# Optimization experiments

Measured on AMD Instinct MI355X. Metric: run time of the kernel, lower is better.

## Reference

```python
import jax, jax.numpy as jnp
import numpy as np

N_NODES = 50000
N_EDGES = 800000
IN_C = 128
OUT_C = 128


def setup_inputs() -> dict:
    key = jax.random.key(0)
    k1, k2, k3 = jax.random.split(key, 3)
    x = jax.random.normal(k1, (N_NODES, IN_C), dtype=jnp.float32)
    edge_index = jax.random.randint(k2, (2, N_EDGES), 0, N_NODES, dtype=jnp.int64)
    weight = jax.random.normal(k3, (IN_C, OUT_C), dtype=jnp.float32) * 0.01
    bias = jnp.zeros((OUT_C,), dtype=jnp.float32)
    return {"x": x, "edge_index": edge_index, "weight": weight, "bias": bias}


def reference(x, edge_index, weight, bias):
    num_nodes = x.shape[0]
    # add self-loops
    loop = jnp.arange(num_nodes, dtype=edge_index.dtype)
    src = jnp.concatenate([edge_index[0], loop])  # [E + N]
    dst = jnp.concatenate([edge_index[1], loop])  # [E + N]
    # in-degree (incl. self-loops) via scatter-add
    deg = jax.ops.segment_sum(jnp.ones_like(dst, dtype=x.dtype), dst,
                              num_segments=num_nodes)
    # deg >= 1 due to self-loops, but guard inf like the original
    deg_inv_sqrt = jnp.where(deg > 0, jax.lax.rsqrt(deg), 0.0)
    norm = deg_inv_sqrt[src] * deg_inv_sqrt[dst]  # [E + N]
    x_transformed = x @ weight  # [N, out_c]
    messages = x_transformed[src] * norm[:, None]  # [E + N, out_c]
    out = jax.ops.segment_sum(messages, dst, num_segments=num_nodes)
    return out + bias
```

## Files before the change

### kernel.cpp

```cpp
#include <hip/hip_runtime.h>

#define C 128
#define CHUNK 3200
#define SLOT 64
#define K4CAP 5120

typedef short bf16x8 __attribute__((ext_vector_type(8)));
typedef float f32x4 __attribute__((ext_vector_type(4)));

__device__ inline unsigned short f2bf(float f) {
    unsigned u = __float_as_uint(f);
    u += 0x7fffu + ((u >> 16) & 1u);
    return (unsigned short)(u >> 16);
}

__device__ inline unsigned pk2bf(float lo, float hi) {
    return (unsigned)f2bf(lo) | ((unsigned)f2bf(hi) << 16);
}

__global__ __launch_bounds__(256) void kA(
        const int* __restrict__ ei, int e,
        int* __restrict__ cnt, unsigned* __restrict__ staging,
        int nblocks, int nbuck,
        const float* __restrict__ W, unsigned short* __restrict__ Wt) {
    int b = blockIdx.x;
    int t = threadIdx.x;
    if (b >= nblocks) {
        int i = (b - nblocks) * 256 + t;
        int nn = i >> 7, k = i & 127;
        Wt[nn * 128 + k] = f2bf(W[k * 128 + nn]);
        return;
    }
    __shared__ int sdst[CHUNK];
    __shared__ int ssrc[CHUNK];
    __shared__ int h[256];
    __shared__ int c[256];
    h[t] = 0;
    __syncthreads();
    int base = b * CHUNK;
    int lim = min(CHUNK, e - base);
    for (int i = t; i < lim; i += 256) {
        int s = ei[base + i];
        int d = ei[e + base + i];
        ssrc[i] = s;
        sdst[i] = d;
        atomicAdd(&h[d >> 8], 1);
    }
    __syncthreads();
    if (t < nbuck) {
        cnt[t * nblocks + b] = h[t];
        c[t] = (t * nblocks + b) * SLOT;
    }
    __syncthreads();
    for (int i = t; i < lim; i += 256) {
        int s = ssrc[i];
        int d = sdst[i];
        int g = d >> 8;
        int pos = atomicAdd(&c[g], 1);
        if (pos < (g * nblocks + b + 1) * SLOT)
            staging[pos] = (unsigned)s | ((unsigned)(d & 255) << 16);
    }
}

__global__ __launch_bounds__(256) void kB(
        const unsigned* __restrict__ staging, const int* __restrict__ cnt,
        int nblocks, int nbuck,
        int2* __restrict__ row_se, float* __restrict__ dis,
        unsigned short* __restrict__ srcs,
        const float* __restrict__ x, const unsigned short* __restrict__ Wt,
        unsigned short* __restrict__ xts, int n) {
    __shared__ unsigned rec[K4CAP];
    __shared__ int sc[256];
    __shared__ int cu[256];
    int b = blockIdx.x, t = threadIdx.x;
    if (b < nbuck) {
        int g = b;
        int segc = (t < nblocks) ? cnt[g * nblocks + t] : 0;
        sc[t] = segc;
        __syncthreads();
        for (int off = 1; off < 256; off <<= 1) {
            int u = (t >= off) ? sc[t - off] : 0;
            __syncthreads();
            sc[t] += u;
            __syncthreads();
        }
        int segbase = sc[t] - segc;
        int total = min(sc[255], K4CAP);
        const unsigned* segp = staging + ((size_t)g * nblocks + t) * SLOT;
        for (int k = 0; k < segc; ++k)
            if (segbase + k < K4CAP) rec[segbase + k] = segp[k];
        __syncthreads();
        sc[t] = 0;
        __syncthreads();
        for (int li = t; li < total; li += 256)
            atomicAdd(&sc[rec[li] >> 16], 1);
        __syncthreads();
        int v = sc[t];
        __syncthreads();
        for (int off = 1; off < 256; off <<= 1) {
            int u = (t >= off) ? sc[t - off] : 0;
            __syncthreads();
            sc[t] += u;
            __syncthreads();
        }
        int excl = sc[t] - v;
        int idx = g * 256 + t;
        int s0 = g * K4CAP;
        if (idx < n) {
            row_se[idx] = make_int2(s0 + excl, s0 + excl + v);
            dis[idx] = rsqrtf((float)(v + 1));
        }
        cu[t] = s0 + excl;
        __syncthreads();
        for (int li = t; li < total; li += 256) {
            unsigned r = rec[li];
            int pos = atomicAdd(&cu[r >> 16], 1);
            srcs[pos] = (unsigned short)(r & 0xffffu);
        }
    } else {
        const int gb = b - nbuck;
        const int lane = t & 63;
        const int wave = t >> 6;
        const int m = lane & 15;
        const int q = lane >> 4;
        const int r0 = gb * 64 + wave * 16;
        const int row = r0 + m;
        const int rowc = (row < n) ? row : (n - 1);

        f32x4 acc[8];
#pragma unroll
        for (int nt = 0; nt < 8; ++nt) acc[nt] = (f32x4){0.f, 0.f, 0.f, 0.f};

#pragma unroll
        for (int kb = 0; kb < 4; ++kb) {
            const int k0 = kb * 32 + q * 8;
            const float4* xp = (const float4*)(x + (size_t)rowc * 128 + k0);
            float4 xa = xp[0];
            float4 xb = xp[1];
            union { unsigned u[4]; bf16x8 v; } af;
            af.u[0] = pk2bf(xa.x, xa.y);
            af.u[1] = pk2bf(xa.z, xa.w);
            af.u[2] = pk2bf(xb.x, xb.y);
            af.u[3] = pk2bf(xb.z, xb.w);
#pragma unroll
            for (int nt = 0; nt < 8; ++nt) {
                bf16x8 bf = *(const bf16x8*)(Wt + (size_t)(nt * 16 + m) * 128 + k0);
                acc[nt] = __builtin_amdgcn_mfma_f32_16x16x32_bf16(af.v, bf, acc[nt], 0, 0, 0);
            }
        }

#pragma unroll
        for (int nt = 0; nt < 8; ++nt) {
            int col = nt * 16 + m;
#pragma unroll
            for (int r = 0; r < 4; ++r) {
                int gr = r0 + q * 4 + r;
                if (gr < n)
                    xts[(size_t)gr * 128 + col] = f2bf(acc[nt][r]);
            }
        }
    }
}

__device__ inline void fma8(float* a, uint4 w, float d) {
    a[0] += __uint_as_float(w.x << 16) * d;
    a[1] += __uint_as_float(w.x & 0xffff0000u) * d;
    a[2] += __uint_as_float(w.y << 16) * d;
    a[3] += __uint_as_float(w.y & 0xffff0000u) * d;
    a[4] += __uint_as_float(w.z << 16) * d;
    a[5] += __uint_as_float(w.z & 0xffff0000u) * d;
    a[6] += __uint_as_float(w.w << 16) * d;
    a[7] += __uint_as_float(w.w & 0xffff0000u) * d;
}

__global__ void gather4(const int2* __restrict__ row_se,
                        const unsigned short* __restrict__ srcs,
                        const unsigned short* __restrict__ xts,
                        const float* __restrict__ dis,
                        const float* __restrict__ bias, float* __restrict__ out, int n) {
    int node = blockIdx.x * 4 + (threadIdx.x >> 6);
    if (node >= n) return;
    int lane = threadIdx.x & 63;
    int e = lane >> 4, q = lane & 15;
    const uint4* x4 = (const uint4*)xts;
    int2 se = row_se[node];
    int end = se.y;
    float dself = dis[node];
    float a0[8] = {0, 0, 0, 0, 0, 0, 0, 0};
    float a1[8] = {0, 0, 0, 0, 0, 0, 0, 0};
    if (e == 0) fma8(a0, x4[node * 16 + q], dself);
    int j = se.x + e;
    for (; j + 4 < end; j += 8) {
        int s0 = srcs[j], s1 = srcs[j + 4];
        float d0 = dis[s0], d1 = dis[s1];
        uint4 m0 = x4[s0 * 16 + q];
        uint4 m1 = x4[s1 * 16 + q];
        fma8(a0, m0, d0);
        fma8(a1, m1, d1);
    }
    if (j < end) {
        int s = srcs[j];
        fma8(a0, x4[s * 16 + q], dis[s]);
    }
#pragma unroll
    for (int i = 0; i < 8; ++i) a0[i] += a1[i];
#pragma unroll
    for (int i = 0; i < 8; ++i) {
        a0[i] += __shfl_xor(a0[i], 16, 64);
        a0[i] += __shfl_xor(a0[i], 32, 64);
    }
    if (e == 0) {
        const float4 b = ((const float4*)bias)[q * 2];
        float4 o;
        o.x = a0[0] * dself + b.x;
        o.y = a0[1] * dself + b.y;
        o.z = a0[2] * dself + b.z;
        o.w = a0[3] * dself + b.w;
        ((float4*)(out + (size_t)node * 128))[q * 2] = o;
    } else if (e == 1) {
        const float4 b = ((const float4*)bias)[q * 2 + 1];
        float4 o;
        o.x = a0[4] * dself + b.x;
        o.y = a0[5] * dself + b.y;
        o.z = a0[6] * dself + b.z;
        o.w = a0[7] * dself + b.w;
        ((float4*)(out + (size_t)node * 128))[q * 2 + 1] = o;
    }
}

extern "C" void kernel_launch(void* const* d_in, const int* in_sizes, int n_in,
                              void* d_out, int out_size, void* d_ws, size_t ws_size,
                              hipStream_t stream) {
    const float* x    = (const float*)d_in[0];
    const int*   ei   = (const int*)d_in[1];
    const float* W    = (const float*)d_in[2];
    const float* bias = (const float*)d_in[3];
    float* out = (float*)d_out;

    const int n = in_sizes[0] / C;
    const int e = in_sizes[1] / 2;
    const int nblocks = (e + CHUNK - 1) / CHUNK;
    const int nbuck = (n + 255) >> 8;
    const int G = (n + 63) / 64;

    char* p = (char*)d_ws;
    auto alloc = [&](size_t bytes) {
        char* r = p;
        p += (bytes + 15) & ~(size_t)15;
        return (void*)r;
    };
    int*      cnt     = (int*)alloc((size_t)nbuck * nblocks * 4);
    unsigned* staging = (unsigned*)alloc((size_t)nbuck * nblocks * SLOT * 4);
    int2*     row_se  = (int2*)alloc((size_t)n * 8);
    float*    dis     = (float*)alloc(n * 4);
    unsigned short* srcs = (unsigned short*)alloc((size_t)nbuck * K4CAP * 2);
    unsigned short* xts  = (unsigned short*)alloc((size_t)n * C * 2);
    unsigned short* Wt   = (unsigned short*)alloc(128 * 128 * 2);

    kA<<<nblocks + 64, 256, 0, stream>>>(ei, e, cnt, staging, nblocks, nbuck,
                                         W, Wt);
    kB<<<nbuck + G, 256, 0, stream>>>(staging, cnt, nblocks, nbuck, row_se,
                                      dis, srcs, x, Wt, xts, n);
    gather4<<<(n + 3) / 4, 256, 0, stream>>>(row_se, srcs, xts, dis, bias, out, n);
}
```

Before: 150.3 us.

## Move GEMM into first kernel with LDS-staged swizzled weights, split bucket finalize

The x@W GEMM blocks now run in the first launch alongside edge bucketing. Each GEMM block converts W to bf16 itself into a swizzled shared-memory tile, so the separate Wt global buffer and its dependency are gone. Bucket finalization becomes its own small kernel that reads staging with vectorized uint4 loads and clamps counts to SLOT. This overlaps the GEMM with the memory-bound scatter and shortens the second stage. The cost is that every GEMM block redundantly converts the full 128x128 weight matrix, and the shared union raises LDS use.

```diff
diff --git a/kernel.cpp b/kernel.cpp
--- a/kernel.cpp
+++ b/kernel.cpp
@@ -18,107 +18,61 @@
     return (unsigned)f2bf(lo) | ((unsigned)f2bf(hi) << 16);
 }
 
-__global__ __launch_bounds__(256) void kA(
+__device__ inline int wt_slot(int nn, int k8) {
+    return (nn * 16 + k8) ^ (nn & 7);
+}
+
+union K1SM {
+    struct { int sdst[CHUNK]; int ssrc[CHUNK]; int h[256]; int c[256]; } ed;
+    bf16x8 wt[2048];
+};
+
+__global__ __launch_bounds__(256) void k1(
         const int* __restrict__ ei, int e,
         int* __restrict__ cnt, unsigned* __restrict__ staging,
         int nblocks, int nbuck,
-        const float* __restrict__ W, unsigned short* __restrict__ Wt) {
+        const float* __restrict__ x, const float* __restrict__ W,
+        unsigned short* __restrict__ xts, int n) {
+    __shared__ K1SM sm;
     int b = blockIdx.x;
     int t = threadIdx.x;
-    if (b >= nblocks) {
-        int i = (b - nblocks) * 256 + t;
-        int nn = i >> 7, k = i & 127;
-        Wt[nn * 128 + k] = f2bf(W[k * 128 + nn]);
-        return;
-    }
-    __shared__ int sdst[CHUNK];
-    __shared__ int ssrc[CHUNK];
-    __shared__ int h[256];
-    __shared__ int c[256];
-    h[t] = 0;
-    __syncthreads();
-    int base = b * CHUNK;
-    int lim = min(CHUNK, e - base);
-    for (int i = t; i < lim; i += 256) {
-        int s = ei[base + i];
-        int d = ei[e + base + i];
-        ssrc[i] = s;
-        sdst[i] = d;
-        atomicAdd(&h[d >> 8], 1);
-    }
-    __syncthreads();
-    if (t < nbuck) {
-        cnt[t * nblocks + b] = h[t];
-        c[t] = (t * nblocks + b) * SLOT;
-    }
-    __syncthreads();
-    for (int i = t; i < lim; i += 256) {
-        int s = ssrc[i];
-        int d = sdst[i];
-        int g = d >> 8;
-        int pos = atomicAdd(&c[g], 1);
-        if (pos < (g * nblocks + b + 1) * SLOT)
-            staging[pos] = (unsigned)s | ((unsigned)(d & 255) << 16);
-    }
-}
-
-__global__ __launch_bounds__(256) void kB(
-        const unsigned* __restrict__ staging, const int* __restrict__ cnt,
-        int nblocks, int nbuck,
-        int2* __restrict__ row_se, float* __restrict__ dis,
-        unsigned short* __restrict__ srcs,
-        const float* __restrict__ x, const unsigned short* __restrict__ Wt,
-        unsigned short* __restrict__ xts, int n) {
-    __shared__ unsigned rec[K4CAP];
-    __shared__ int sc[256];
-    __shared__ int cu[256];
-    int b = blockIdx.x, t = threadIdx.x;
-    if (b < nbuck) {
-        int g = b;
-        int segc = (t < nblocks) ? cnt[g * nblocks + t] : 0;
-        sc[t] = segc;
-        __syncthreads();
-        for (int off = 1; off < 256; off <<= 1) {
-            int u = (t >= off) ? sc[t - off] : 0;
-            __syncthreads();
-            sc[t] += u;
-            __syncthreads();
-        }
-        int segbase = sc[t] - segc;
-        int total = min(sc[255], K4CAP);
-        const unsigned* segp = staging + ((size_t)g * nblocks + t) * SLOT;
-        for (int k = 0; k < segc; ++k)
-            if (segbase + k < K4CAP) rec[segbase + k] = segp[k];
-        __syncthreads();
-        sc[t] = 0;
-        __syncthreads();
-        for (int li = t; li < total; li += 256)
-            atomicAdd(&sc[rec[li] >> 16], 1);
-        __syncthreads();
-        int v = sc[t];
-        __syncthreads();
-        for (int off = 1; off < 256; off <<= 1) {
-            int u = (t >= off) ? sc[t - off] : 0;
-            __syncthreads();
-            sc[t] += u;
-            __syncthreads();
-        }
-        int excl = sc[t] - v;
-        int idx = g * 256 + t;
-        int s0 = g * K4CAP;
-        if (idx < n) {
-            row_se[idx] = make_int2(s0 + excl, s0 + excl + v);
-            dis[idx] = rsqrtf((float)(v + 1));
-        }
-        cu[t] = s0 + excl;
-        __syncthreads();
-        for (int li = t; li < total; li += 256) {
-            unsigned r = rec[li];
-            int pos = atomicAdd(&cu[r >> 16], 1);
-            srcs[pos] = (unsigned short)(r & 0xffffu);
+    if (b < nblocks) {
+        sm.ed.h[t] = 0;
+        __syncthreads();
+        int base = b * CHUNK;
+        int lim = min(CHUNK, e - base);
+        for (int i = t; i < lim; i += 256) {
+            int s = ei[base + i];
+            int d = ei[e + base + i];
+            sm.ed.ssrc[i] = s;
+            sm.ed.sdst[i] = d;
+            atomicAdd(&sm.ed.h[d >> 8], 1);
+        }
+        __syncthreads();
+        if (t < nbuck) {
+            cnt[t * nblocks + b] = sm.ed.h[t];
+            sm.ed.c[t] = (t * nblocks + b) * SLOT;
+        }
+        __syncthreads();
+        for (int i = t; i < lim; i += 256) {
+            int s = sm.ed.ssrc[i];
+            int d = sm.ed.sdst[i];
+            int g = d >> 8;
+            int pos = atomicAdd(&sm.ed.c[g], 1);
+            if (pos < (g * nblocks + b + 1) * SLOT)
+                staging[pos] = (unsigned)s | ((unsigned)(d & 255) << 16);
         }
     } else {
-        const int gb = b - nbuck;
+        unsigned* sw32 = (unsigned*)sm.wt;
+        for (int ii = t; ii < 8192; ii += 256) {
+            int nn = ii & 127;
+            int k = (ii >> 7) * 2;
+            unsigned pk = pk2bf(W[k * 128 + nn], W[(k + 1) * 128 + nn]);
+            sw32[wt_slot(nn, k >> 3) * 4 + ((k & 7) >> 1)] = pk;
+        }
+        __syncthreads();
+
+        const int gb = b - nblocks;
         const int lane = t & 63;
         const int wave = t >> 6;
         const int m = lane & 15;
@@ -144,7 +98,7 @@
             af.u[3] = pk2bf(xb.z, xb.w);
 #pragma unroll
             for (int nt = 0; nt < 8; ++nt) {
-                bf16x8 bf = *(const bf16x8*)(Wt + (size_t)(nt * 16 + m) * 128 + k0);
+                bf16x8 bf = sm.wt[wt_slot(nt * 16 + m, kb * 4 + q)];
                 acc[nt] = __builtin_amdgcn_mfma_f32_16x16x32_bf16(af.v, bf, acc[nt], 0, 0, 0);
             }
         }
@@ -159,6 +113,65 @@
                     xts[(size_t)gr * 128 + col] = f2bf(acc[nt][r]);
             }
         }
+    }
+}
+
+__global__ __launch_bounds__(256) void kfin(
+        const unsigned* __restrict__ staging, const int* __restrict__ cnt,
+        int nblocks, int nbuck,
+        int2* __restrict__ row_se, float* __restrict__ dis,
+        unsigned short* __restrict__ srcs, int n) {
+    __shared__ unsigned rec[K4CAP];
+    __shared__ int sc[256];
+    __shared__ int cu[256];
+    int g = blockIdx.x, t = threadIdx.x;
+    int segc = (t < nblocks) ? min(cnt[g * nblocks + t], SLOT) : 0;
+    sc[t] = segc;
+    __syncthreads();
+    for (int off = 1; off < 256; off <<= 1) {
+        int u = (t >= off) ? sc[t - off] : 0;
+        __syncthreads();
+        sc[t] += u;
+        __syncthreads();
+    }
+    int segbase = sc[t] - segc;
+    int total = min(sc[255], K4CAP);
+    const unsigned* segp = staging + ((size_t)g * nblocks + t) * SLOT;
+    for (int k = 0; k < segc; k += 4) {
+        uint4 w = *(const uint4*)(segp + k);
+        int bd = segbase + k;
+        if (bd < K4CAP) rec[bd] = w.x;
+        if (k + 1 < segc && bd + 1 < K4CAP) rec[bd + 1] = w.y;
+        if (k + 2 < segc && bd + 2 < K4CAP) rec[bd + 2] = w.z;
+        if (k + 3 < segc && bd + 3 < K4CAP) rec[bd + 3] = w.w;
+    }
+    __syncthreads();
+    sc[t] = 0;
+    __syncthreads();
+    for (int li = t; li < total; li += 256)
+        atomicAdd(&sc[rec[li] >> 16], 1);
+    __syncthreads();
+    int v = sc[t];
+    __syncthreads();
+    for (int off = 1; off < 256; off <<= 1) {
+        int u = (t >= off) ? sc[t - off] : 0;
+        __syncthreads();
+        sc[t] += u;
+        __syncthreads();
+    }
+    int excl = sc[t] - v;
+    int idx = g * 256 + t;
+    int s0 = g * K4CAP;
+    if (idx < n) {
+        row_se[idx] = make_int2(s0 + excl, s0 + excl + v);
+        dis[idx] = rsqrtf((float)(v + 1));
+    }
+    cu[t] = s0 + excl;
+    __syncthreads();
+    for (int li = t; li < total; li += 256) {
+        unsigned r = rec[li];
+        int pos = atomicAdd(&cu[r >> 16], 1);
+        srcs[pos] = (unsigned short)(r & 0xffffu);
     }
 }
 
@@ -255,11 +268,10 @@
     float*    dis     = (float*)alloc(n * 4);
     unsigned short* srcs = (unsigned short*)alloc((size_t)nbuck * K4CAP * 2);
     unsigned short* xts  = (unsigned short*)alloc((size_t)n * C * 2);
-    unsigned short* Wt   = (unsigned short*)alloc(128 * 128 * 2);
-
-    kA<<<nblocks + 64, 256, 0, stream>>>(ei, e, cnt, staging, nblocks, nbuck,
-                                         W, Wt);
-    kB<<<nbuck + G, 256, 0, stream>>>(staging, cnt, nblocks, nbuck, row_se,
-                                      dis, srcs, x, Wt, xts, n);
+
+    k1<<<nblocks + G, 256, 0, stream>>>(ei, e, cnt, staging, nblocks, nbuck,
+                                        x, W, xts, n);
+    kfin<<<nbuck, 256, 0, stream>>>(staging, cnt, nblocks, nbuck, row_se,
+                                    dis, srcs, n);
     gather4<<<(n + 3) / 4, 256, 0, stream>>>(row_se, srcs, xts, dis, bias, out, n);
 }
```

New measurement: 143.9 us. 4.3% less time.
